# Performance work log

Hardware: AMD Instinct MI355X
Metric: run time of the kernel (lower is better)

## Reference

```python
import jax, jax.numpy as jnp
import numpy as np

LR = 0.001  # fixed self.lr in ODE_Vanilla

B, T, I, H, C = 128, 256, 256, 1024, 10


def setup_inputs() -> dict:
    key = jax.random.key(0)
    ks = jax.random.split(key, 6)
    stdv = 1.0 / np.sqrt(H)
    u = lambda k, shape: jax.random.uniform(k, shape, jnp.float32, -stdv, stdv)
    return {
        "X": jax.random.normal(ks[0], (B, T, I), jnp.float32),
        "hidden": jnp.zeros((B, H), jnp.float32),
        "alpha": jnp.zeros((1,), jnp.float32),  # alpha is excluded from re-init, stays 0.0
        "b": u(ks[1], (H,)),
        "Wh": u(ks[2], (H, H)),
        "Wx": u(ks[3], (I, H)),
        "fc_w": u(ks[4], (H, C)),
        "fc_b": u(ks[5], (C,)),
    }


def reference(X, hidden, alpha, b, Wh, Wx, fc_w, fc_b):
    # X: (B, T, I) -> scan over time-major (T, B, I)
    a = alpha[0]
    Xt = jnp.transpose(X, (1, 0, 2))

    def step(h, x):
        # phi = relu(h @ Wh + x @ Wx + b)
        phi = jax.nn.relu(h @ Wh + x @ Wx + b)
        mask = (phi > 0).astype(h.dtype)
        # st = a*I - diag(mask) @ Wh; grad = st @ (a*h - phi)
        # collapses to: a*v - mask * (v @ Wh^T), with v = a*h - phi
        v = a * h - phi
        grad = a * v - mask * (v @ Wh.T)
        h_new = h - LR * grad
        return h_new, h_new

    h_final, outs = jax.lax.scan(step, hidden, Xt)  # outs: (T, B, H)
    # last_layer (single_output=False, class task): FC over all timesteps
    out = jnp.transpose(outs, (1, 0, 2)) @ fc_w + fc_b  # (B, T, C)
    return out.reshape(-1, out.shape[-1]), h_final
```

## Files before the change

### kernel.cpp

```cpp
#include <hip/hip_runtime.h>


constexpr int Bsz = 128, Tn = 256, In = 256, Hn = 1024, Cn = 10;
constexpr float LR = 0.001f;

__global__ __launch_bounds__(256) void k_transpose(const float* __restrict__ W,
                                                   float* __restrict__ WT) {
  __shared__ float tile[32][33];
  const int bx = blockIdx.x * 32, by = blockIdx.y * 32;
  const int tx = threadIdx.x & 31, ty = threadIdx.x >> 5;
#pragma unroll
  for (int dy = 0; dy < 32; dy += 8)
    tile[ty + dy][tx] = W[(size_t)(by + ty + dy) * Hn + bx + tx];
  __syncthreads();
#pragma unroll
  for (int dy = 0; dy < 32; dy += 8)
    WT[(size_t)(bx + ty + dy) * Hn + by + tx] = tile[tx][ty + dy];
}

__global__ __launch_bounds__(256) void k_init(float* __restrict__ out,
                                              const float* __restrict__ fc_b,
                                              float* __restrict__ h_cur,
                                              const float* __restrict__ hidden) {
  const int i = blockIdx.x * blockDim.x + threadIdx.x;
  if (i < Bsz * Tn * Cn) out[i] = fc_b[i % Cn];
  if (i < Bsz * Hn) h_cur[i] = hidden[i];
}

__device__ __forceinline__ void fma4(float4& a, float s, const float4& w) {
  a.x = fmaf(s, w.x, a.x);
  a.y = fmaf(s, w.y, a.y);
  a.z = fmaf(s, w.z, a.z);
  a.w = fmaf(s, w.w, a.w);
}

__device__ __forceinline__ float4 shfl4(float4 v, int m) {
  v.x = __shfl_xor(v.x, m, 64);
  v.y = __shfl_xor(v.y, m, 64);
  v.z = __shfl_xor(v.z, m, 64);
  v.w = __shfl_xor(v.w, m, 64);
  return v;
}

__device__ __forceinline__ float4 add4(float4 a, float4 b) {
  return make_float4(a.x + b.x, a.y + b.y, a.z + b.z, a.w + b.w);
}

__global__ __launch_bounds__(256) void k_xw(const float* __restrict__ X,
                                            const float* __restrict__ Wx,
                                            const float* __restrict__ bias,
                                            float* __restrict__ xw) {
  const int nt = blockIdx.x & 15, mt = blockIdx.x >> 4;
  const int t = mt >> 1, b0 = (mt & 1) * 64;
  const int cl = threadIdx.x & 15, rg = threadIdx.x >> 4;
  const int col = nt * 64 + cl * 4;
  const int row = b0 + rg * 4;
  float4 acc0 = {0, 0, 0, 0}, acc1 = {0, 0, 0, 0}, acc2 = {0, 0, 0, 0},
         acc3 = {0, 0, 0, 0};
  const size_t xstride = (size_t)Tn * In;
  const float* xp = X + ((size_t)row * Tn + t) * In;
  const float* wp = Wx + col;
#pragma unroll 2
  for (int k = 0; k < In; k += 4) {
    const float4 x0 = *(const float4*)(xp + k);
    const float4 x1 = *(const float4*)(xp + xstride + k);
    const float4 x2 = *(const float4*)(xp + 2 * xstride + k);
    const float4 x3 = *(const float4*)(xp + 3 * xstride + k);
    const float4 w0 = *(const float4*)(wp + (size_t)k * Hn);
    const float4 w1 = *(const float4*)(wp + (size_t)(k + 1) * Hn);
    const float4 w2 = *(const float4*)(wp + (size_t)(k + 2) * Hn);
    const float4 w3 = *(const float4*)(wp + (size_t)(k + 3) * Hn);
    fma4(acc0, x0.x, w0); fma4(acc0, x0.y, w1); fma4(acc0, x0.z, w2); fma4(acc0, x0.w, w3);
    fma4(acc1, x1.x, w0); fma4(acc1, x1.y, w1); fma4(acc1, x1.z, w2); fma4(acc1, x1.w, w3);
    fma4(acc2, x2.x, w0); fma4(acc2, x2.y, w1); fma4(acc2, x2.z, w2); fma4(acc2, x2.w, w3);
    fma4(acc3, x3.x, w0); fma4(acc3, x3.y, w1); fma4(acc3, x3.z, w2); fma4(acc3, x3.w, w3);
  }
  const float4 b4 = *(const float4*)(bias + col);
  float4 o[4] = {acc0, acc1, acc2, acc3};
#pragma unroll
  for (int i = 0; i < 4; i++) {
    float4 v = o[i];
    v.x += b4.x; v.y += b4.y; v.z += b4.z; v.w += b4.w;
    *(float4*)(xw + ((size_t)t * Bsz + row + i) * Hn + col) = v;
  }
}

__device__ __forceinline__ void gemm8g(const float* __restrict__ rows,
                                       const float* __restrict__ W, int kk,
                                       int col, float4 acc[8]) {
#pragma unroll
  for (int q = 0; q < 4; q++) {
    const int k = 4 * kk + 256 * q;
    const float* Wp = W + (size_t)k * Hn + col;
    const float4 w0 = *(const float4*)(Wp);
    const float4 w1 = *(const float4*)(Wp + Hn);
    const float4 w2 = *(const float4*)(Wp + 2 * Hn);
    const float4 w3 = *(const float4*)(Wp + 3 * Hn);
#pragma unroll
    for (int r = 0; r < 8; r++) {
      const float4 h4 = *(const float4*)(rows + (size_t)r * Hn + k);
      fma4(acc[r], h4.x, w0);
      fma4(acc[r], h4.y, w1);
      fma4(acc[r], h4.z, w2);
      fma4(acc[r], h4.w, w3);
    }
  }
}

__device__ __forceinline__ void reduce_vs(float4 acc[8], int c4, int ksw,
                                          int wv, float (*part)[8][16]) {
  const bool u1 = ksw & 1;
#pragma unroll
  for (int i = 0; i < 4; i++) {
    const float4 snd = u1 ? acc[i] : acc[i + 4];
    const float4 kp = u1 ? acc[i + 4] : acc[i];
    acc[i] = add4(kp, shfl4(snd, 4));
  }
  const bool u2 = ksw & 2;
#pragma unroll
  for (int i = 0; i < 2; i++) {
    const float4 snd = u2 ? acc[i] : acc[i + 2];
    const float4 kp = u2 ? acc[i + 2] : acc[i];
    acc[i] = add4(kp, shfl4(snd, 8));
  }
  const bool u3 = ksw & 4;
  {
    const float4 snd = u3 ? acc[0] : acc[1];
    const float4 kp = u3 ? acc[1] : acc[0];
    acc[0] = add4(kp, shfl4(snd, 16));
  }
  const bool u4 = ksw & 8;
  float sx = u4 ? acc[0].x : acc[0].z;
  float sy = u4 ? acc[0].y : acc[0].w;
  const float kx = u4 ? acc[0].z : acc[0].x;
  const float ky = u4 ? acc[0].w : acc[0].y;
  sx = __shfl_xor(sx, 32, 64);
  sy = __shfl_xor(sy, 32, 64);
  const int r_own = ((ksw & 1) << 2) | (ksw & 2) | ((ksw >> 2) & 1);
  const int c_own = 4 * c4 + (u4 ? 2 : 0);
  *(float2*)&part[wv][r_own][c_own] = make_float2(kx + sx, ky + sy);
}

template <int PRE>
__global__ __launch_bounds__(256, 4) void k_phase1(
    const float* __restrict__ h, const float* __restrict__ X,
    const float* __restrict__ Wh, const float* __restrict__ Wx,
    const float* __restrict__ bias, const float* __restrict__ alpha,
    const float* __restrict__ xw, float* __restrict__ v_out, int t) {
  __shared__ float part[4][8][16];
  const int ct = blockIdx.x & 63, rt = blockIdx.x >> 6;
  const int c0 = ct * 16, r0 = rt * 8;
  const int tid = threadIdx.x;
  const int c4 = tid & 3, kk = tid >> 2;
  const int col = c0 + 4 * c4;
  const int wv = tid >> 6, ksw = (tid & 63) >> 2;
  const float* hbase = h + (size_t)r0 * Hn;

  float a1 = 0.f, hv = 0.f;
  if (tid < 128) {
    const int r = tid >> 4, c = tid & 15;
    a1 = PRE ? xw[((size_t)t * Bsz + r0 + r) * Hn + c0 + c] : bias[c0 + c];
    hv = hbase[(size_t)r * Hn + c0 + c];
  }

  float4 acc[8];
#pragma unroll
  for (int r = 0; r < 8; r++) acc[r] = {0.f, 0.f, 0.f, 0.f};
  gemm8g(hbase, Wh, kk, col, acc);
  if (!PRE) {
    const int kx = 4 * kk;
    const float* Wp = Wx + (size_t)kx * Hn + col;
    const float4 w0 = *(const float4*)(Wp);
    const float4 w1 = *(const float4*)(Wp + Hn);
    const float4 w2 = *(const float4*)(Wp + 2 * Hn);
    const float4 w3 = *(const float4*)(Wp + 3 * Hn);
#pragma unroll
    for (int r = 0; r < 8; r++) {
      const float4 x4 =
          *(const float4*)(X + ((size_t)(r0 + r) * Tn + t) * In + kx);
      fma4(acc[r], x4.x, w0);
      fma4(acc[r], x4.y, w1);
      fma4(acc[r], x4.z, w2);
      fma4(acc[r], x4.w, w3);
    }
  }
  reduce_vs(acc, c4, ksw, wv, part);
  __syncthreads();
  if (tid < 128) {
    const int r = tid >> 4, c = tid & 15;
    const float u =
        part[0][r][c] + part[1][r][c] + part[2][r][c] + part[3][r][c];
    const float av = alpha[0];
    v_out[(size_t)(r0 + r) * Hn + c0 + c] = av * hv - fmaxf(u + a1, 0.f);
  }
}

__global__ __launch_bounds__(256, 4) void k_phase2(
    float* __restrict__ h, const float* __restrict__ v_in,
    const float* __restrict__ WT, const float* __restrict__ alpha,
    const float* __restrict__ fc_w, float* __restrict__ out,
    float* __restrict__ hfin, int t, int last) {
  __shared__ float part[4][8][16];
  __shared__ float hn_s[8][16];
  const int ct = blockIdx.x & 63, rt = blockIdx.x >> 6;
  const int c0 = ct * 16, r0 = rt * 8;
  const int tid = threadIdx.x;
  const int c4 = tid & 3, kk = tid >> 2;
  const int col = c0 + 4 * c4;
  const int wv = tid >> 6, ksw = (tid & 63) >> 2;
  const float* vbase = v_in + (size_t)r0 * Hn;

  float hv = 0.f, vv = 0.f;
  if (tid < 128) {
    const int r = tid >> 4, c = tid & 15;
    hv = h[(size_t)(r0 + r) * Hn + c0 + c];
    vv = vbase[(size_t)r * Hn + c0 + c];
  }

  float4 acc[8];
#pragma unroll
  for (int r = 0; r < 8; r++) acc[r] = {0.f, 0.f, 0.f, 0.f};
  gemm8g(vbase, WT, kk, col, acc);
  reduce_vs(acc, c4, ksw, wv, part);
  __syncthreads();
  if (tid < 128) {
    const int r = tid >> 4, c = tid & 15;
    const float u =
        part[0][r][c] + part[1][r][c] + part[2][r][c] + part[3][r][c];
    const float av = alpha[0];
    const size_t hoff = (size_t)(r0 + r) * Hn + c0 + c;
    const float hn = hv - LR * (av * vv - ((av * hv - vv) > 0.f ? u : 0.f));
    h[hoff] = hn;
    if (last) hfin[hoff] = hn;
    hn_s[r][c] = hn;
  }
  __syncthreads();
  if (tid < 80) {
    const int rr = tid / 10, c = tid % 10;
    float s = 0.f;
#pragma unroll
    for (int jj = 0; jj < 16; jj++)
      s += hn_s[rr][jj] * fc_w[(size_t)(c0 + jj) * Cn + c];
    atomicAdd(&out[((size_t)(r0 + rr) * Tn + t) * Cn + c], s);
  }
}

extern "C" void kernel_launch(void* const* d_in, const int* in_sizes, int n_in,
                              void* d_out, int out_size, void* d_ws, size_t ws_size,
                              hipStream_t stream) {
  const float* X      = (const float*)d_in[0];
  const float* hidden = (const float*)d_in[1];
  const float* alpha  = (const float*)d_in[2];
  const float* bias   = (const float*)d_in[3];
  const float* Wh     = (const float*)d_in[4];
  const float* Wx     = (const float*)d_in[5];
  const float* fc_w   = (const float*)d_in[6];
  const float* fc_b   = (const float*)d_in[7];
  float* out  = (float*)d_out;
  float* hfin = out + (size_t)Bsz * Tn * Cn;

  char* ws = (char*)d_ws;
  float* WhT   = (float*)ws;
  float* h_cur = WhT + (size_t)Hn * Hn;
  float* v_buf = h_cur + (size_t)Bsz * Hn;
  float* XW    = v_buf + (size_t)Bsz * Hn;
  const size_t need =
      ((size_t)Hn * Hn + 2 * (size_t)Bsz * Hn + (size_t)Bsz * Tn * Hn) *
      sizeof(float);
  const bool pre = ws_size >= need;

  k_transpose<<<dim3(32, 32), 256, 0, stream>>>(Wh, WhT);
  k_init<<<(Bsz * Tn * Cn + 255) / 256, 256, 0, stream>>>(out, fc_b, h_cur,
                                                          hidden);
  if (pre) k_xw<<<8192, 256, 0, stream>>>(X, Wx, bias, XW);
  for (int t = 0; t < Tn; t++) {
    if (pre)
      k_phase1<1><<<1024, 256, 0, stream>>>(h_cur, X, Wh, Wx, bias, alpha, XW,
                                            v_buf, t);
    else
      k_phase1<0><<<1024, 256, 0, stream>>>(h_cur, X, Wh, Wx, bias, alpha, XW,
                                            v_buf, t);
    k_phase2<<<1024, 256, 0, stream>>>(h_cur, v_buf, WhT, alpha, fc_w, out,
                                       hfin, t, t == Tn - 1);
  }
}
```

Measured before the change: 5.953 ms.

## Stage weight slabs in LDS and double row tile per block in recurrent GEMMs

Each recurrent-step block now handles 16 rows instead of 8 with 512 threads split into two row groups. Both groups share one weight slab that is staged through swizzled LDS, so each weight element is fetched from global memory once per block rather than once per row group. The next slab is prefetched into registers while the current one is consumed. This halves global weight traffic per step, at the cost of extra barriers and fewer blocks (512 instead of 1024), which reduces parallelism.

```diff
diff --git a/kernel.cpp b/kernel.cpp
--- a/kernel.cpp
+++ b/kernel.cpp
@@ -85,27 +85,7 @@
   }
 }
 
-__device__ __forceinline__ void gemm8g(const float* __restrict__ rows,
-                                       const float* __restrict__ W, int kk,
-                                       int col, float4 acc[8]) {
-#pragma unroll
-  for (int q = 0; q < 4; q++) {
-    const int k = 4 * kk + 256 * q;
-    const float* Wp = W + (size_t)k * Hn + col;
-    const float4 w0 = *(const float4*)(Wp);
-    const float4 w1 = *(const float4*)(Wp + Hn);
-    const float4 w2 = *(const float4*)(Wp + 2 * Hn);
-    const float4 w3 = *(const float4*)(Wp + 3 * Hn);
-#pragma unroll
-    for (int r = 0; r < 8; r++) {
-      const float4 h4 = *(const float4*)(rows + (size_t)r * Hn + k);
-      fma4(acc[r], h4.x, w0);
-      fma4(acc[r], h4.y, w1);
-      fma4(acc[r], h4.z, w2);
-      fma4(acc[r], h4.w, w3);
-    }
-  }
-}
+#define WSLOT(krow, cq) (((krow) << 2) + ((cq) ^ ((krow)&3)))
 
 __device__ __forceinline__ void reduce_vs(float4 acc[8], int c4, int ksw,
                                           int wv, float (*part)[8][16]) {
@@ -141,23 +121,66 @@
   *(float2*)&part[wv][r_own][c_own] = make_float2(kx + sx, ky + sy);
 }
 
+__device__ __forceinline__ void gemm16_lds(const float* __restrict__ rows,
+                                           const float* __restrict__ W,
+                                           int c0, int tid, float4* wslab,
+                                           float4 acc[8]) {
+  const int g = tid >> 8;
+  const int c4 = tid & 3, kk = (tid >> 2) & 63;
+  const float* rbase = rows + (size_t)(g * 8) * Hn;
+  const int f0 = tid, f1 = tid + 512;
+  const int kr0 = f0 >> 2, cq0 = f0 & 3, kr1 = f1 >> 2, cq1 = f1 & 3;
+  const float* g0 = W + (size_t)kr0 * Hn + c0 + 4 * cq0;
+  const float* g1 = W + (size_t)kr1 * Hn + c0 + 4 * cq1;
+  const int s0i = WSLOT(kr0, cq0), s1i = WSLOT(kr1, cq1);
+
+  float4 s0 = *(const float4*)(g0);
+  float4 s1 = *(const float4*)(g1);
+#pragma unroll
+  for (int q = 0; q < 4; q++) {
+    __syncthreads();
+    wslab[s0i] = s0;
+    wslab[s1i] = s1;
+    if (q < 3) {
+      s0 = *(const float4*)(g0 + (size_t)256 * (q + 1) * Hn);
+      s1 = *(const float4*)(g1 + (size_t)256 * (q + 1) * Hn);
+    }
+    __syncthreads();
+    const int klocal = 4 * kk;
+    const float4 w0 = wslab[WSLOT(klocal, c4)];
+    const float4 w1 = wslab[WSLOT(klocal + 1, c4)];
+    const float4 w2 = wslab[WSLOT(klocal + 2, c4)];
+    const float4 w3 = wslab[WSLOT(klocal + 3, c4)];
+    const int k = klocal + 256 * q;
+#pragma unroll
+    for (int r = 0; r < 8; r++) {
+      const float4 h4 = *(const float4*)(rbase + (size_t)r * Hn + k);
+      fma4(acc[r], h4.x, w0);
+      fma4(acc[r], h4.y, w1);
+      fma4(acc[r], h4.z, w2);
+      fma4(acc[r], h4.w, w3);
+    }
+  }
+}
+
 template <int PRE>
-__global__ __launch_bounds__(256, 4) void k_phase1(
+__global__ __launch_bounds__(512, 4) void k_phase1(
     const float* __restrict__ h, const float* __restrict__ X,
     const float* __restrict__ Wh, const float* __restrict__ Wx,
     const float* __restrict__ bias, const float* __restrict__ alpha,
     const float* __restrict__ xw, float* __restrict__ v_out, int t) {
-  __shared__ float part[4][8][16];
+  __shared__ float4 wslab[1024];
+  __shared__ float part[2][4][8][16];
   const int ct = blockIdx.x & 63, rt = blockIdx.x >> 6;
-  const int c0 = ct * 16, r0 = rt * 8;
+  const int c0 = ct * 16, r0 = rt * 16;
   const int tid = threadIdx.x;
-  const int c4 = tid & 3, kk = tid >> 2;
-  const int col = c0 + 4 * c4;
-  const int wv = tid >> 6, ksw = (tid & 63) >> 2;
+  const int g = tid >> 8, c4 = tid & 3, kk = (tid >> 2) & 63;
+  const int wvh = (tid >> 6) & 3, ksw = (tid & 63) >> 2;
   const float* hbase = h + (size_t)r0 * Hn;
+  const float av = alpha[0];
 
   float a1 = 0.f, hv = 0.f;
-  if (tid < 128) {
+  if (tid < 256) {
     const int r = tid >> 4, c = tid & 15;
     a1 = PRE ? xw[((size_t)t * Bsz + r0 + r) * Hn + c0 + c] : bias[c0 + c];
     hv = hbase[(size_t)r * Hn + c0 + c];
@@ -166,52 +189,56 @@
   float4 acc[8];
 #pragma unroll
   for (int r = 0; r < 8; r++) acc[r] = {0.f, 0.f, 0.f, 0.f};
-  gemm8g(hbase, Wh, kk, col, acc);
+  gemm16_lds(hbase, Wh + c0, c0 - c0, tid, wslab, acc);
   if (!PRE) {
     const int kx = 4 * kk;
-    const float* Wp = Wx + (size_t)kx * Hn + col;
+    const float* Wp = Wx + (size_t)kx * Hn + c0 + 4 * c4;
     const float4 w0 = *(const float4*)(Wp);
     const float4 w1 = *(const float4*)(Wp + Hn);
     const float4 w2 = *(const float4*)(Wp + 2 * Hn);
     const float4 w3 = *(const float4*)(Wp + 3 * Hn);
+    const float* rbase = hbase;
 #pragma unroll
     for (int r = 0; r < 8; r++) {
       const float4 x4 =
-          *(const float4*)(X + ((size_t)(r0 + r) * Tn + t) * In + kx);
+          *(const float4*)(X + ((size_t)(r0 + 8 * g + r) * Tn + t) * In + kx);
       fma4(acc[r], x4.x, w0);
       fma4(acc[r], x4.y, w1);
       fma4(acc[r], x4.z, w2);
       fma4(acc[r], x4.w, w3);
     }
-  }
-  reduce_vs(acc, c4, ksw, wv, part);
+    (void)rbase;
+  }
+  reduce_vs(acc, c4, ksw, wvh, part[g]);
   __syncthreads();
-  if (tid < 128) {
+  if (tid < 256) {
     const int r = tid >> 4, c = tid & 15;
-    const float u =
-        part[0][r][c] + part[1][r][c] + part[2][r][c] + part[3][r][c];
-    const float av = alpha[0];
+    const int g2 = r >> 3, rl = r & 7;
+    const float u = part[g2][0][rl][c] + part[g2][1][rl][c] +
+                    part[g2][2][rl][c] + part[g2][3][rl][c];
     v_out[(size_t)(r0 + r) * Hn + c0 + c] = av * hv - fmaxf(u + a1, 0.f);
   }
 }
 
-__global__ __launch_bounds__(256, 4) void k_phase2(
+__global__ __launch_bounds__(512, 4) void k_phase2(
     float* __restrict__ h, const float* __restrict__ v_in,
     const float* __restrict__ WT, const float* __restrict__ alpha,
     const float* __restrict__ fc_w, float* __restrict__ out,
     float* __restrict__ hfin, int t, int last) {
-  __shared__ float part[4][8][16];
-  __shared__ float hn_s[8][16];
+  __shared__ float4 wslab[1024];
+  __shared__ float part[2][4][8][16];
+  __shared__ float hn_s[16][16];
   const int ct = blockIdx.x & 63, rt = blockIdx.x >> 6;
-  const int c0 = ct * 16, r0 = rt * 8;
+  const int c0 = ct * 16, r0 = rt * 16;
   const int tid = threadIdx.x;
-  const int c4 = tid & 3, kk = tid >> 2;
-  const int col = c0 + 4 * c4;
-  const int wv = tid >> 6, ksw = (tid & 63) >> 2;
+  const int g = tid >> 8, c4 = tid & 3, kk = (tid >> 2) & 63;
+  const int wvh = (tid >> 6) & 3, ksw = (tid & 63) >> 2;
   const float* vbase = v_in + (size_t)r0 * Hn;
+  const float av = alpha[0];
+  (void)g; (void)kk; (void)c4;
 
   float hv = 0.f, vv = 0.f;
-  if (tid < 128) {
+  if (tid < 256) {
     const int r = tid >> 4, c = tid & 15;
     hv = h[(size_t)(r0 + r) * Hn + c0 + c];
     vv = vbase[(size_t)r * Hn + c0 + c];
@@ -220,14 +247,14 @@
   float4 acc[8];
 #pragma unroll
   for (int r = 0; r < 8; r++) acc[r] = {0.f, 0.f, 0.f, 0.f};
-  gemm8g(vbase, WT, kk, col, acc);
-  reduce_vs(acc, c4, ksw, wv, part);
+  gemm16_lds(vbase, WT + c0, 0, tid, wslab, acc);
+  reduce_vs(acc, tid & 3, ksw, wvh, part[tid >> 8]);
   __syncthreads();
-  if (tid < 128) {
+  if (tid < 256) {
     const int r = tid >> 4, c = tid & 15;
-    const float u =
-        part[0][r][c] + part[1][r][c] + part[2][r][c] + part[3][r][c];
-    const float av = alpha[0];
+    const int g2 = r >> 3, rl = r & 7;
+    const float u = part[g2][0][rl][c] + part[g2][1][rl][c] +
+                    part[g2][2][rl][c] + part[g2][3][rl][c];
     const size_t hoff = (size_t)(r0 + r) * Hn + c0 + c;
     const float hn = hv - LR * (av * vv - ((av * hv - vv) > 0.f ? u : 0.f));
     h[hoff] = hn;
@@ -235,7 +262,7 @@
     hn_s[r][c] = hn;
   }
   __syncthreads();
-  if (tid < 80) {
+  if (tid < 160) {
     const int rr = tid / 10, c = tid % 10;
     float s = 0.f;
 #pragma unroll
@@ -275,12 +302,12 @@
   if (pre) k_xw<<<8192, 256, 0, stream>>>(X, Wx, bias, XW);
   for (int t = 0; t < Tn; t++) {
     if (pre)
-      k_phase1<1><<<1024, 256, 0, stream>>>(h_cur, X, Wh, Wx, bias, alpha, XW,
-                                            v_buf, t);
+      k_phase1<1><<<512, 512, 0, stream>>>(h_cur, X, Wh, Wx, bias, alpha, XW,
+                                           v_buf, t);
     else
-      k_phase1<0><<<1024, 256, 0, stream>>>(h_cur, X, Wh, Wx, bias, alpha, XW,
-                                            v_buf, t);
-    k_phase2<<<1024, 256, 0, stream>>>(h_cur, v_buf, WhT, alpha, fc_w, out,
-                                       hfin, t, t == Tn - 1);
-  }
-}
+      k_phase1<0><<<512, 512, 0, stream>>>(h_cur, X, Wh, Wx, bias, alpha, XW,
+                                           v_buf, t);
+    k_phase2<<<512, 512, 0, stream>>>(h_cur, v_buf, WhT, alpha, fc_w, out,
+                                      hfin, t, t == Tn - 1);
+  }
+}
```

After: 6.481 ms. 8.9% more time.
